# Kernel optimization log

Hardware: AMD Instinct MI355X
Metric: run time of the kernel (lower is better)

Reference implementation:

```python
import jax, jax.numpy as jnp
import numpy as np

N, D = 16384, 256
T = 0.5
C = 100


def setup_inputs() -> dict:
    key = jax.random.key(0)
    x = jax.random.normal(key, (N, D), dtype=jnp.float32)
    # L2-normalize rows (standard for contrastive embeddings; also keeps
    # exp(sim/T) in fp32 range, matching the module's intended use)
    x = x / jnp.linalg.norm(x, axis=1, keepdims=True)
    return {"x": x}


def reference(x) -> jnp.ndarray:
    # sim[i,j] = <x_i, x_j> / T ; loss = (1/C) * sum_i log(sum_j exp(sim[i,j]))
    sim = jnp.exp(jnp.matmul(x, x.T) / T)          # [N, N]
    row = jnp.log(jnp.sum(sim, axis=1))            # [N]
    return jnp.sum(row) / C                        # scalar
```

## Files before the change

kernel.cpp:

```cpp
#include <hip/hip_runtime.h>
#include <hip/hip_bf16.h>


#define N_ROWS 16384
#define KD     256
#define BM     256
#define BN     64
#define NSPLIT 8
#define COLS_PER (N_ROWS / NSPLIT)
#define NITER    (COLS_PER / BN)

#define SCALE_SQRT 1.6986436f

typedef short short8 __attribute__((ext_vector_type(8)));
typedef float f32x4  __attribute__((ext_vector_type(4)));

typedef __attribute__((address_space(3))) void       lds_void;
typedef const __attribute__((address_space(1))) void gm_void;

__device__ __forceinline__ float fast_exp2(float x) {
#if __has_builtin(__builtin_amdgcn_exp2f)
    return __builtin_amdgcn_exp2f(x);
#else
    return exp2f(x);
#endif
}

__device__ __forceinline__ void gll16(const void* g, void* l) {
    __builtin_amdgcn_global_load_lds((gm_void*)g, (lds_void*)l, 16, 0, 0);
}

__global__ void convert_kernel(const float* __restrict__ x, unsigned short* __restrict__ xb) {
    int i = (blockIdx.x * 256 + threadIdx.x) * 4;
    float4 v = *(const float4*)(x + i);
    ushort4 o;
    {
        unsigned int u;
        u = __float_as_uint(v.x * SCALE_SQRT); u += 0x7fff + ((u >> 16) & 1); o.x = (unsigned short)(u >> 16);
        u = __float_as_uint(v.y * SCALE_SQRT); u += 0x7fff + ((u >> 16) & 1); o.y = (unsigned short)(u >> 16);
        u = __float_as_uint(v.z * SCALE_SQRT); u += 0x7fff + ((u >> 16) & 1); o.z = (unsigned short)(u >> 16);
        u = __float_as_uint(v.w * SCALE_SQRT); u += 0x7fff + ((u >> 16) & 1); o.w = (unsigned short)(u >> 16);
    }
    *(ushort4*)(xb + i) = o;
}

__global__ __launch_bounds__(256, 2)
void simloss_main(const unsigned short* __restrict__ xb, float* __restrict__ partial) {
    __shared__ __align__(128) char smem[65536];

    const int tid  = threadIdx.x;
    const int lane = tid & 63;
    const int w    = tid >> 6;
    const int bx   = blockIdx.x;
    const int split = bx & 7;
    const int rb    = bx >> 3;
    const int r0      = rb * BM;
    const int colBase = split * COLS_PER;

    const int l15 = lane & 15;
    const int lg  = lane >> 4;

    short8 afrag[4][8];
    #pragma unroll
    for (int m = 0; m < 4; ++m) {
        const unsigned short* arow = xb + (size_t)(r0 + w * 64 + m * 16 + l15) * KD + lg * 8;
        #pragma unroll
        for (int kt = 0; kt < 8; ++kt)
            afrag[m][kt] = *(const short8*)(arow + kt * 32);
    }
    #pragma unroll
    for (int m = 0; m < 4; ++m)
        #pragma unroll
        for (int kt = 0; kt < 8; ++kt)
            asm volatile("" : "+v"(afrag[m][kt]));

    const unsigned short* bsrc0 = xb + (size_t)(colBase + w * 16 + l15) * KD + lg * 8;
    char* const ldst0 = smem + (w * 8) * 1024;

    auto stageB = [&](int buf, int it2) {
        const unsigned short* s = bsrc0 + (size_t)it2 * (BN * KD);
        char* dst = ldst0 + buf * 32768;
        #pragma unroll
        for (int kt = 0; kt < 8; ++kt)
            gll16(s + kt * 32, dst + kt * 1024);
    };

    float rowsum[4][4] = {{0.f}};

    stageB(0, 0);

    for (int it = 0; it < NITER; ++it) {
        const int cur = it & 1;
        if (it + 1 < NITER) {
            stageB(cur ^ 1, it + 1);
            asm volatile("s_waitcnt vmcnt(8)" ::: "memory");
        } else {
            asm volatile("s_waitcnt vmcnt(0)" ::: "memory");
        }
        __builtin_amdgcn_s_barrier();
        asm volatile("" ::: "memory");

        const char* bbase = smem + cur * 32768;
        #pragma unroll
        for (int ct = 0; ct < 4; ++ct) {
            short8 bfrag[8];
            #pragma unroll
            for (int kt = 0; kt < 8; ++kt)
                bfrag[kt] = *(const short8*)(bbase + (ct * 8 + kt) * 1024 + lane * 16);
            f32x4 acc[4];
            #pragma unroll
            for (int m = 0; m < 4; ++m) acc[m] = (f32x4){0.f, 0.f, 0.f, 0.f};
            #pragma unroll
            for (int kt = 0; kt < 8; ++kt)
                #pragma unroll
                for (int m = 0; m < 4; ++m)
                    acc[m] = __builtin_amdgcn_mfma_f32_16x16x32_bf16(afrag[m][kt], bfrag[kt], acc[m], 0, 0, 0);
            #pragma unroll
            for (int m = 0; m < 4; ++m)
                #pragma unroll
                for (int r = 0; r < 4; ++r)
                    rowsum[m][r] += fast_exp2(acc[m][r]);
        }

        asm volatile("" ::: "memory");
        __builtin_amdgcn_s_barrier();
        asm volatile("" ::: "memory");
    }

    #pragma unroll
    for (int m = 0; m < 4; ++m)
        #pragma unroll
        for (int r = 0; r < 4; ++r) {
            float v = rowsum[m][r];
            v += __shfl_xor(v, 1);
            v += __shfl_xor(v, 2);
            v += __shfl_xor(v, 4);
            v += __shfl_xor(v, 8);
            if (l15 == 0) {
                int row = r0 + w * 64 + m * 16 + lg * 4 + r;
                partial[split * N_ROWS + row] = v;
            }
        }
}

__global__ void zero_out(float* __restrict__ out) { out[0] = 0.f; }

__global__ void finalize_kernel(const float* __restrict__ partial, float* __restrict__ out) {
    int i = blockIdx.x * 256 + threadIdx.x;
    float s = 0.f;
    #pragma unroll
    for (int p = 0; p < NSPLIT; ++p) s += partial[p * N_ROWS + i];
    float v = logf(s);
    #pragma unroll
    for (int off = 1; off < 64; off <<= 1) v += __shfl_xor(v, off);
    __shared__ float red[4];
    if ((threadIdx.x & 63) == 0) red[threadIdx.x >> 6] = v;
    __syncthreads();
    if (threadIdx.x == 0)
        atomicAdd(out, (red[0] + red[1] + red[2] + red[3]) * 0.01f);
}

extern "C" void kernel_launch(void* const* d_in, const int* in_sizes, int n_in,
                              void* d_out, int out_size, void* d_ws, size_t ws_size,
                              hipStream_t stream) {
    const float* x = (const float*)d_in[0];
    unsigned short* xb = (unsigned short*)d_ws;
    float* partial = (float*)((char*)d_ws + (size_t)N_ROWS * KD * 2);
    float* out = (float*)d_out;

    convert_kernel<<<(N_ROWS * KD) / (256 * 4), 256, 0, stream>>>(x, xb);
    simloss_main<<<(N_ROWS / BM) * NSPLIT, 256, 0, stream>>>(xb, partial);
    zero_out<<<1, 1, 0, stream>>>(out);
    finalize_kernel<<<N_ROWS / 256, 256, 0, stream>>>(partial, out);
}
```

Measured before the change: 171.4 us.

## Exploit Gram matrix symmetry: compute lower-triangle tiles with row and column atomics

Replaces the row-split grid with a 64x64 tile grid where only lower-triangle tiles do work; each off-diagonal tile adds its exp sums to both its rows and its columns via atomicAdd, halving matmul and exp work. Zeroing of the accumulator and output is folded into the conversion kernel, removing a launch, and the finalize no longer sums splits. In exchange each block reloads A fragments for only 256 columns, issues many global atomics, and half the launched blocks exit immediately.

```diff
diff --git a/kernel.cpp b/kernel.cpp
--- a/kernel.cpp
+++ b/kernel.cpp
@@ -6,9 +6,8 @@
 #define KD     256
 #define BM     256
 #define BN     64
-#define NSPLIT 8
-#define COLS_PER (N_ROWS / NSPLIT)
-#define NITER    (COLS_PER / BN)
+#define NT     (N_ROWS / BM)
+#define NITER  (BM / BN)
 
 #define SCALE_SQRT 1.6986436f
 
@@ -30,8 +29,12 @@
     __builtin_amdgcn_global_load_lds((gm_void*)g, (lds_void*)l, 16, 0, 0);
 }
 
-__global__ void convert_kernel(const float* __restrict__ x, unsigned short* __restrict__ xb) {
-    int i = (blockIdx.x * 256 + threadIdx.x) * 4;
+__global__ void convert_kernel(const float* __restrict__ x, unsigned short* __restrict__ xb,
+                               float* __restrict__ partial, float* __restrict__ out) {
+    const int bx = blockIdx.x, tid = threadIdx.x;
+    if (bx < N_ROWS / 256) partial[bx * 256 + tid] = 0.f;
+    if (bx == N_ROWS / 256 && tid == 0) out[0] = 0.f;
+    int i = (bx * 256 + tid) * 4;
     float4 v = *(const float4*)(x + i);
     ushort4 o;
     {
@@ -46,16 +49,19 @@
 
 __global__ __launch_bounds__(256, 2)
 void simloss_main(const unsigned short* __restrict__ xb, float* __restrict__ partial) {
+    const int bx = blockIdx.x;
+    const int rb = bx >> 6;
+    const int cb = bx & 63;
+    if (cb > rb) return;
+    const bool diag = (rb == cb);
+
     __shared__ __align__(128) char smem[65536];
 
     const int tid  = threadIdx.x;
     const int lane = tid & 63;
     const int w    = tid >> 6;
-    const int bx   = blockIdx.x;
-    const int split = bx & 7;
-    const int rb    = bx >> 3;
-    const int r0      = rb * BM;
-    const int colBase = split * COLS_PER;
+    const int r0 = rb * BM;
+    const int c0 = cb * BM;
 
     const int l15 = lane & 15;
     const int lg  = lane >> 4;
@@ -74,7 +80,7 @@
         for (int kt = 0; kt < 8; ++kt)
             asm volatile("" : "+v"(afrag[m][kt]));
 
-    const unsigned short* bsrc0 = xb + (size_t)(colBase + w * 16 + l15) * KD + lg * 8;
+    const unsigned short* bsrc0 = xb + (size_t)(c0 + w * 16 + l15) * KD + lg * 8;
     char* const ldst0 = smem + (w * 8) * 1024;
 
     auto stageB = [&](int buf, int it2) {
@@ -89,6 +95,7 @@
 
     stageB(0, 0);
 
+    #pragma unroll
     for (int it = 0; it < NITER; ++it) {
         const int cur = it & 1;
         if (it + 1 < NITER) {
@@ -115,11 +122,21 @@
                 #pragma unroll
                 for (int m = 0; m < 4; ++m)
                     acc[m] = __builtin_amdgcn_mfma_f32_16x16x32_bf16(afrag[m][kt], bfrag[kt], acc[m], 0, 0, 0);
+            float csum = 0.f;
             #pragma unroll
             for (int m = 0; m < 4; ++m)
                 #pragma unroll
-                for (int r = 0; r < 4; ++r)
-                    rowsum[m][r] += fast_exp2(acc[m][r]);
+                for (int r = 0; r < 4; ++r) {
+                    float e = fast_exp2(acc[m][r]);
+                    rowsum[m][r] += e;
+                    csum += e;
+                }
+            if (!diag) {
+                csum += __shfl_xor(csum, 16);
+                csum += __shfl_xor(csum, 32);
+                if (lg == 0)
+                    atomicAdd(partial + c0 + it * BN + ct * 16 + l15, csum);
+            }
         }
 
         asm volatile("" ::: "memory");
@@ -136,21 +153,14 @@
             v += __shfl_xor(v, 2);
             v += __shfl_xor(v, 4);
             v += __shfl_xor(v, 8);
-            if (l15 == 0) {
-                int row = r0 + w * 64 + m * 16 + lg * 4 + r;
-                partial[split * N_ROWS + row] = v;
-            }
+            if (l15 == 0)
+                atomicAdd(partial + r0 + w * 64 + m * 16 + lg * 4 + r, v);
         }
 }
 
-__global__ void zero_out(float* __restrict__ out) { out[0] = 0.f; }
-
 __global__ void finalize_kernel(const float* __restrict__ partial, float* __restrict__ out) {
     int i = blockIdx.x * 256 + threadIdx.x;
-    float s = 0.f;
-    #pragma unroll
-    for (int p = 0; p < NSPLIT; ++p) s += partial[p * N_ROWS + i];
-    float v = logf(s);
+    float v = logf(partial[i]);
     #pragma unroll
     for (int off = 1; off < 64; off <<= 1) v += __shfl_xor(v, off);
     __shared__ float red[4];
@@ -168,8 +178,7 @@
     float* partial = (float*)((char*)d_ws + (size_t)N_ROWS * KD * 2);
     float* out = (float*)d_out;
 
-    convert_kernel<<<(N_ROWS * KD) / (256 * 4), 256, 0, stream>>>(x, xb);
-    simloss_main<<<(N_ROWS / BM) * NSPLIT, 256, 0, stream>>>(xb, partial);
-    zero_out<<<1, 1, 0, stream>>>(out);
+    convert_kernel<<<(N_ROWS * KD) / (256 * 4), 256, 0, stream>>>(x, xb, partial, out);
+    simloss_main<<<NT * NT, 256, 0, stream>>>(xb, partial);
     finalize_kernel<<<N_ROWS / 256, 256, 0, stream>>>(partial, out);
 }
```

Result: slower. 407.5 us (+137.8%).
